# Kernel tuning notes

Measured on AMD Instinct MI355X. Metric: run time of the kernel, lower is better.

Reference implementation:

```python
import jax, jax.numpy as jnp
import numpy as np

EPS = 1e-6  # VNLeakyReLU eps
NORM_EPS = 1e-12  # F.normalize default eps
NEG_SLOPE = 0.2


def _normalize(v):
    # matches torch F.normalize(p=2, dim=-1): v / max(||v||, eps)
    n = jnp.linalg.norm(v, axis=-1, keepdims=True)
    return v / jnp.maximum(n, NORM_EPS)


def _bgs_extended(d6s):
    # d6s: [B,N,D,3,2] -> rotation matrices [B,N,D,3,3] (columns b1,b2,b3)
    b1 = _normalize(d6s[..., 0])
    a2 = d6s[..., 1]
    proj = jnp.sum(b1 * a2, axis=-1, keepdims=True) * b1
    b2 = _normalize(a2 - proj)
    b3 = jnp.cross(b1, b2)
    return jnp.stack([b1, b2, b3], axis=-1)


def setup_inputs() -> dict:
    key = jax.random.key(0)
    kX, kJ, kA, kB, kC, kW = jax.random.split(key, 6)
    B, N, Din, Dout = 8, 4096, 128, 256
    return {
        "X": jax.random.normal(kX, (B, N, Din, 3), dtype=jnp.float32),
        "J": jax.random.normal(kJ, (B, N, Din, 3, 2), dtype=jnp.float32),
        "Amat": jax.random.normal(kA, (Dout, Din), dtype=jnp.float32),
        "Bmat": jax.random.normal(kB, (Dout, Din), dtype=jnp.float32),
        "Cmat": jax.random.normal(kC, (Dout, Din), dtype=jnp.float32),
        "Wdir": jax.random.normal(kW, (Dout, Dout), dtype=jnp.float32),
        "device": 0,
    }


def reference(X, J, Amat, Bmat, Cmat, Wdir, device):
    # ---- Affine_Linear_Abla_wocomplex ----
    R = _bgs_extended(J)  # [B,N,D,3,3]
    # get_rtx(k, RT, X) = sum_j R[...,j,k] * X[...,j]; stacking k=0,1,2 gives:
    a_term = jnp.einsum('bndjk,bndj->bndk', R, X)  # [B,N,D,3]
    # Y = A@a + B@a + C@a == (A+B+C)@a  (einsum 'fe,bcei->bcfi')
    Y = jnp.einsum('fe,bnei->bnfi', Amat + Bmat + Cmat, a_term)  # [B,N,F,3]
    # ---- permute(0,2,3,1) -> [B, F, 3, N] ----
    x = jnp.transpose(Y, (0, 2, 3, 1))
    # ---- VNLeakyReLU ----
    d = jnp.einsum('oc,bcin->boin', Wdir, x)
    dot = jnp.sum(x * d, axis=2, keepdims=True)
    mask = (dot >= 0).astype(x.dtype)
    d_norm_sq = jnp.sum(d * d, axis=2, keepdims=True)
    x_out = NEG_SLOPE * x + (1 - NEG_SLOPE) * (
        mask * x + (1 - mask) * (x - dot / (d_norm_sq + EPS) * d)
    )
    return x_out  # [B, F, 3, N]
```

## Files before the change

kernel.cpp:

```cpp
#include <hip/hip_runtime.h>

#define TT 16
#define NBLK 2048
#define LDA 136

typedef short s16x8 __attribute__((ext_vector_type(8)));
typedef float f32x4 __attribute__((ext_vector_type(4)));

#define SCHED_FENCE() __builtin_amdgcn_sched_barrier(0)

__device__ __forceinline__ unsigned short f2bf(float f) {
  union { float f; unsigned u; } v; v.f = f;
  unsigned r = v.u + 0x7FFFu + ((v.u >> 16) & 1u);
  return (unsigned short)(r >> 16);
}
__device__ __forceinline__ float bf2f(unsigned short h) {
  union { unsigned u; float f; } v; v.u = ((unsigned)h) << 16;
  return v.f;
}
__device__ __forceinline__ void split2(float x, unsigned short& h, unsigned short& m) {
  h = f2bf(x);
  m = f2bf(x - bf2f(h));
}

__global__ __launch_bounds__(256) void prep1_kernel(
    const float* __restrict__ A, const float* __restrict__ Bm,
    const float* __restrict__ C,
    float* __restrict__ M3f,
    unsigned short* __restrict__ M3h, unsigned short* __restrict__ M3m) {
  int tid = blockIdx.x * 256 + threadIdx.x;
  float s = A[tid] + Bm[tid] + C[tid];
  M3f[tid] = s;
  unsigned short h, m;
  split2(s, h, m);
  M3h[tid] = h; M3m[tid] = m;
}

__global__ __launch_bounds__(256) void prep2_kernel(
    const float* __restrict__ W, const float* __restrict__ M3f,
    unsigned short* __restrict__ WMh, unsigned short* __restrict__ WMm) {
  __shared__ float wrow[256];
  __shared__ float part[128];
  const int o = blockIdx.x;
  const int t = threadIdx.x;
  const int e = t & 127;
  const int h = t >> 7;
  wrow[t] = W[o * 256 + t];
  __syncthreads();
  float dot = 0.f;
  const int c0 = h * 128;
  #pragma unroll 8
  for (int c = c0; c < c0 + 128; ++c) dot += wrow[c] * M3f[c * 128 + e];
  if (h) part[e] = dot;
  __syncthreads();
  if (!h) {
    float d = dot + part[e];
    unsigned short hh, mm;
    split2(d, hh, mm);
    WMh[o * 128 + e] = hh; WMm[o * 128 + e] = mm;
  }
}

#define B1LOADS(slot, ks) { \
  b1h[slot][0] = *(const s16x8*)(M3h + fB + (ks) * 32); \
  b1m[slot][0] = *(const s16x8*)(M3m + fB + (ks) * 32); \
  b1h[slot][1] = *(const s16x8*)(M3h + fB + 2048 + (ks) * 32); \
  b1m[slot][1] = *(const s16x8*)(M3m + fB + 2048 + (ks) * 32); }

#define WMLOADS(slot, ks) { \
  wmh[slot][0] = *(const s16x8*)(WMh + fB + (ks) * 32); \
  wmm[slot][0] = *(const s16x8*)(WMm + fB + (ks) * 32); \
  wmh[slot][1] = *(const s16x8*)(WMh + fB + 2048 + (ks) * 32); \
  wmm[slot][1] = *(const s16x8*)(WMm + fB + 2048 + (ks) * 32); }

#define GSTEPS(slot, ks) { \
  const int e0 = (ks) * 32 + quad * 8; \
  _Pragma("unroll") \
  for (int mt = 0; mt < 3; ++mt) { \
    s16x8 ah = *(const s16x8*)(aTh + (mt * 16 + nl) * LDA + e0); \
    s16x8 am = *(const s16x8*)(aTm + (mt * 16 + nl) * LDA + e0); \
    _Pragma("unroll") \
    for (int nt = 0; nt < 2; ++nt) { \
      f32x4 a1 = acc1[mt][nt]; \
      f32x4 a2 = acc2[mt][nt]; \
      a1 = __builtin_amdgcn_mfma_f32_16x16x32_bf16(ah, b1h[slot][nt], a1, 0, 0, 0); \
      a2 = __builtin_amdgcn_mfma_f32_16x16x32_bf16(ah, wmh[slot][nt], a2, 0, 0, 0); \
      a1 = __builtin_amdgcn_mfma_f32_16x16x32_bf16(ah, b1m[slot][nt], a1, 0, 0, 0); \
      a2 = __builtin_amdgcn_mfma_f32_16x16x32_bf16(ah, wmm[slot][nt], a2, 0, 0, 0); \
      a1 = __builtin_amdgcn_mfma_f32_16x16x32_bf16(am, b1h[slot][nt], a1, 0, 0, 0); \
      a2 = __builtin_amdgcn_mfma_f32_16x16x32_bf16(am, wmh[slot][nt], a2, 0, 0, 0); \
      acc1[mt][nt] = a1; acc2[mt][nt] = a2; \
    } \
  } }

__global__ __launch_bounds__(512, 3) void affine_vnrelu_mfma(
    const float* __restrict__ X, const float* __restrict__ J,
    const unsigned short* __restrict__ M3h, const unsigned short* __restrict__ M3m,
    const unsigned short* __restrict__ WMh, const unsigned short* __restrict__ WMm,
    float* __restrict__ out) {
  __shared__ unsigned short smem[2 * 48 * LDA];
  unsigned short* aTh = smem;
  unsigned short* aTm = smem + 48 * LDA;

  const int tid = threadIdx.x;
  const int lane = tid & 63;
  const int w = tid >> 6;
  const int quad = lane >> 4;
  const int nl = lane & 15;
  const long g0 = (long)blockIdx.x * TT;
  const int b = (int)(g0 >> 12);
  const int n0 = (int)(g0 & 4095);
  const int f0 = w * 32;
  const int fB = (f0 + nl) * 128 + quad * 8;
  const f32x4 zz = {0.f, 0.f, 0.f, 0.f};

  s16x8 b1h[2][2], b1m[2][2];
  s16x8 wmh[2][2], wmm[2][2];
  B1LOADS(0, 0); WMLOADS(0, 0);
  SCHED_FENCE();

  {
    int t = tid >> 5;
    int dch0 = (tid & 31) * 4;
    const float* Xp = X + ((g0 + t) * 128 + dch0) * 3;
    const float* Jp = J + ((g0 + t) * 128 + dch0) * 6;
    float xf[12], jf[24];
    #pragma unroll
    for (int q = 0; q < 3; ++q) *(float4*)(xf + 4 * q) = ((const float4*)Xp)[q];
    #pragma unroll
    for (int q = 0; q < 6; ++q) *(float4*)(jf + 4 * q) = ((const float4*)Jp)[q];

    unsigned short hs[3][4], ms[3][4];
    #pragma unroll
    for (int e = 0; e < 4; ++e) {
      float x0 = xf[3 * e], x1 = xf[3 * e + 1], x2 = xf[3 * e + 2];
      float j0 = jf[6 * e],     j1 = jf[6 * e + 1], j2 = jf[6 * e + 2];
      float j3 = jf[6 * e + 3], j4 = jf[6 * e + 4], j5 = jf[6 * e + 5];
      float c00 = j0, c01 = j2, c02 = j4;
      float a20 = j1, a21 = j3, a22 = j5;
      float nsq1 = c00 * c00 + c01 * c01 + c02 * c02;
      float inv1 = __builtin_amdgcn_rsqf(fmaxf(nsq1, 1e-24f));
      float b10 = c00 * inv1, b11 = c01 * inv1, b12 = c02 * inv1;
      float pr = b10 * a20 + b11 * a21 + b12 * a22;
      float u0 = a20 - pr * b10, u1 = a21 - pr * b11, u2 = a22 - pr * b12;
      float nsq2 = u0 * u0 + u1 * u1 + u2 * u2;
      float inv2 = __builtin_amdgcn_rsqf(fmaxf(nsq2, 1e-24f));
      float b20 = u0 * inv2, b21 = u1 * inv2, b22 = u2 * inv2;
      float b30 = b11 * b22 - b12 * b21;
      float b31 = b12 * b20 - b10 * b22;
      float b32 = b10 * b21 - b11 * b20;
      split2(b10 * x0 + b11 * x1 + b12 * x2, hs[0][e], ms[0][e]);
      split2(b20 * x0 + b21 * x1 + b22 * x2, hs[1][e], ms[1][e]);
      split2(b30 * x0 + b31 * x1 + b32 * x2, hs[2][e], ms[2][e]);
    }
    #pragma unroll
    for (int i = 0; i < 3; ++i) {
      short4 vh, vm;
      vh.x = hs[i][0]; vh.y = hs[i][1]; vh.z = hs[i][2]; vh.w = hs[i][3];
      vm.x = ms[i][0]; vm.y = ms[i][1]; vm.z = ms[i][2]; vm.w = ms[i][3];
      int ro = (i * 16 + t) * LDA + dch0;
      *(short4*)(aTh + ro) = vh;
      *(short4*)(aTm + ro) = vm;
    }
  }
  __syncthreads();

  f32x4 acc1[3][2], acc2[3][2];
  #pragma unroll
  for (int mt = 0; mt < 3; ++mt)
    #pragma unroll
    for (int nt = 0; nt < 2; ++nt) { acc1[mt][nt] = zz; acc2[mt][nt] = zz; }

  B1LOADS(1, 1); WMLOADS(1, 1);
  SCHED_FENCE();
  GSTEPS(0, 0);
  B1LOADS(0, 2); WMLOADS(0, 2);
  SCHED_FENCE();
  GSTEPS(1, 1);
  B1LOADS(1, 3); WMLOADS(1, 3);
  SCHED_FENCE();
  GSTEPS(0, 2);
  GSTEPS(1, 3);

  #pragma unroll
  for (int nt = 0; nt < 2; ++nt) {
    int f = f0 + nt * 16 + nl;
    float* ob = out + ((long)(b * 256 + f) * 3) * 4096 + n0 + quad * 4;
    float o[3][4];
    #pragma unroll
    for (int r = 0; r < 4; ++r) {
      float x0 = acc1[0][nt][r], x1 = acc1[1][nt][r], x2 = acc1[2][nt][r];
      float d0 = acc2[0][nt][r], d1 = acc2[1][nt][r], d2 = acc2[2][nt][r];
      float dot = x0 * d0 + x1 * d1 + x2 * d2;
      float dn = d0 * d0 + d1 * d1 + d2 * d2;
      float s = (dot < 0.0f) ? (0.8f * dot * __builtin_amdgcn_rcpf(dn + 1e-6f))
                             : 0.0f;
      o[0][r] = x0 - s * d0;
      o[1][r] = x1 - s * d1;
      o[2][r] = x2 - s * d2;
    }
    #pragma unroll
    for (int i = 0; i < 3; ++i)
      *(float4*)(ob + ((long)i * 4096)) = make_float4(o[i][0], o[i][1], o[i][2], o[i][3]);
  }
}

extern "C" void kernel_launch(void* const* d_in, const int* in_sizes, int n_in,
                              void* d_out, int out_size, void* d_ws, size_t ws_size,
                              hipStream_t stream) {
  const float* X = (const float*)d_in[0];
  const float* J = (const float*)d_in[1];
  const float* A = (const float*)d_in[2];
  const float* B = (const float*)d_in[3];
  const float* C = (const float*)d_in[4];
  const float* W = (const float*)d_in[5];
  unsigned short* M3h = (unsigned short*)d_ws;
  unsigned short* M3m = M3h + 128 * 256;
  unsigned short* WMh = M3m + 128 * 256;
  unsigned short* WMm = WMh + 128 * 256;
  float* M3f = (float*)(WMm + 128 * 256);
  float* out = (float*)d_out;

  prep1_kernel<<<128, 256, 0, stream>>>(A, B, C, M3f, M3h, M3m);
  prep2_kernel<<<256, 256, 0, stream>>>(W, M3f, WMh, WMm);
  affine_vnrelu_mfma<<<NBLK, 512, 0, stream>>>(
      X, J, M3h, M3m, WMh, WMm, out);
}
```

Before: 280.1 us.

## Make GEMM kernel persistent over 8 tiles with prefetched X/J loads

Each block now processes 8 consecutive 16-point tiles instead of one, with a grid of 256 blocks. The X and J loads for the next tile are issued before the current tile's MFMA work so their latency overlaps compute. Launch bounds drop to 2 blocks per SM to make room for the extra prefetch registers. The costs are fewer resident waves, extra barriers between tiles, and a grid of 256 blocks that may leave CUs idle on a 256-CU part at only 2 waves of work per block.

Result: no change. 278.5 us (-0.6%).

```diff
diff --git a/kernel.cpp b/kernel.cpp
--- a/kernel.cpp
+++ b/kernel.cpp
@@ -1,7 +1,8 @@
 #include <hip/hip_runtime.h>
 
 #define TT 16
-#define NBLK 2048
+#define NBLK 256
+#define NTILE 8
 #define LDA 136
 
 typedef short s16x8 __attribute__((ext_vector_type(8)));
@@ -93,7 +94,49 @@
     } \
   } }
 
-__global__ __launch_bounds__(512, 3) void affine_vnrelu_mfma(
+#define LOADXJ(g0t) { \
+  const float* Xp = X + (((g0t) + tA) * 128 + dch0) * 3; \
+  const float* Jp = J + (((g0t) + tA) * 128 + dch0) * 6; \
+  _Pragma("unroll") \
+  for (int q = 0; q < 3; ++q) *(float4*)(xf + 4 * q) = ((const float4*)Xp)[q]; \
+  _Pragma("unroll") \
+  for (int q = 0; q < 6; ++q) *(float4*)(jf + 4 * q) = ((const float4*)Jp)[q]; }
+
+#define GSPROC() { \
+  unsigned short hs[3][4], ms[3][4]; \
+  _Pragma("unroll") \
+  for (int e = 0; e < 4; ++e) { \
+    float x0 = xf[3 * e], x1 = xf[3 * e + 1], x2 = xf[3 * e + 2]; \
+    float j0 = jf[6 * e],     j1 = jf[6 * e + 1], j2 = jf[6 * e + 2]; \
+    float j3 = jf[6 * e + 3], j4 = jf[6 * e + 4], j5 = jf[6 * e + 5]; \
+    float c00 = j0, c01 = j2, c02 = j4; \
+    float a20 = j1, a21 = j3, a22 = j5; \
+    float nsq1 = c00 * c00 + c01 * c01 + c02 * c02; \
+    float inv1 = __builtin_amdgcn_rsqf(fmaxf(nsq1, 1e-24f)); \
+    float b10 = c00 * inv1, b11 = c01 * inv1, b12 = c02 * inv1; \
+    float pr = b10 * a20 + b11 * a21 + b12 * a22; \
+    float u0 = a20 - pr * b10, u1 = a21 - pr * b11, u2 = a22 - pr * b12; \
+    float nsq2 = u0 * u0 + u1 * u1 + u2 * u2; \
+    float inv2 = __builtin_amdgcn_rsqf(fmaxf(nsq2, 1e-24f)); \
+    float b20 = u0 * inv2, b21 = u1 * inv2, b22 = u2 * inv2; \
+    float b30 = b11 * b22 - b12 * b21; \
+    float b31 = b12 * b20 - b10 * b22; \
+    float b32 = b10 * b21 - b11 * b20; \
+    split2(b10 * x0 + b11 * x1 + b12 * x2, hs[0][e], ms[0][e]); \
+    split2(b20 * x0 + b21 * x1 + b22 * x2, hs[1][e], ms[1][e]); \
+    split2(b30 * x0 + b31 * x1 + b32 * x2, hs[2][e], ms[2][e]); \
+  } \
+  _Pragma("unroll") \
+  for (int i = 0; i < 3; ++i) { \
+    short4 vh, vm; \
+    vh.x = hs[i][0]; vh.y = hs[i][1]; vh.z = hs[i][2]; vh.w = hs[i][3]; \
+    vm.x = ms[i][0]; vm.y = ms[i][1]; vm.z = ms[i][2]; vm.w = ms[i][3]; \
+    int ro = (i * 16 + tA) * LDA + dch0; \
+    *(short4*)(aTh + ro) = vh; \
+    *(short4*)(aTm + ro) = vm; \
+  } }
+
+__global__ __launch_bounds__(512, 2) void affine_vnrelu_mfma(
     const float* __restrict__ X, const float* __restrict__ J,
     const unsigned short* __restrict__ M3h, const unsigned short* __restrict__ M3m,
     const unsigned short* __restrict__ WMh, const unsigned short* __restrict__ WMm,
@@ -107,101 +150,80 @@
   const int w = tid >> 6;
   const int quad = lane >> 4;
   const int nl = lane & 15;
-  const long g0 = (long)blockIdx.x * TT;
-  const int b = (int)(g0 >> 12);
-  const int n0 = (int)(g0 & 4095);
   const int f0 = w * 32;
   const int fB = (f0 + nl) * 128 + quad * 8;
+  const int tA = tid >> 5;
+  const int dch0 = (tid & 31) * 4;
   const f32x4 zz = {0.f, 0.f, 0.f, 0.f};
 
   s16x8 b1h[2][2], b1m[2][2];
   s16x8 wmh[2][2], wmm[2][2];
+  float xf[12], jf[24];
+
+  const long gbase = (long)blockIdx.x * NTILE * TT;
+
+  LOADXJ(gbase);
   B1LOADS(0, 0); WMLOADS(0, 0);
   SCHED_FENCE();
-
-  {
-    int t = tid >> 5;
-    int dch0 = (tid & 31) * 4;
-    const float* Xp = X + ((g0 + t) * 128 + dch0) * 3;
-    const float* Jp = J + ((g0 + t) * 128 + dch0) * 6;
-    float xf[12], jf[24];
+  GSPROC();
+  __syncthreads();
+
+  for (int it = 0; it < NTILE; ++it) {
+    const long g0c = gbase + (long)it * TT;
+
+    if (it + 1 < NTILE) { LOADXJ(g0c + TT); }
+    SCHED_FENCE();
+
+    f32x4 acc1[3][2], acc2[3][2];
     #pragma unroll
-    for (int q = 0; q < 3; ++q) *(float4*)(xf + 4 * q) = ((const float4*)Xp)[q];
-    #pragma unroll
-    for (int q = 0; q < 6; ++q) *(float4*)(jf + 4 * q) = ((const float4*)Jp)[q];
-
-    unsigned short hs[3][4], ms[3][4];
-    #pragma unroll
-    for (int e = 0; e < 4; ++e) {
-      float x0 = xf[3 * e], x1 = xf[3 * e + 1], x2 = xf[3 * e + 2];
-      float j0 = jf[6 * e],     j1 = jf[6 * e + 1], j2 = jf[6 * e + 2];
-      float j3 = jf[6 * e + 3], j4 = jf[6 * e + 4], j5 = jf[6 * e + 5];
-      float c00 = j0, c01 = j2, c02 = j4;
-      float a20 = j1, a21 = j3, a22 = j5;
-      float nsq1 = c00 * c00 + c01 * c01 + c02 * c02;
-      float inv1 = __builtin_amdgcn_rsqf(fmaxf(nsq1, 1e-24f));
-      float b10 = c00 * inv1, b11 = c01 * inv1, b12 = c02 * inv1;
-      float pr = b10 * a20 + b11 * a21 + b12 * a22;
-      float u0 = a20 - pr * b10, u1 = a21 - pr * b11, u2 = a22 - pr * b12;
-      float nsq2 = u0 * u0 + u1 * u1 + u2 * u2;
-      float inv2 = __builtin_amdgcn_rsqf(fmaxf(nsq2, 1e-24f));
-      float b20 = u0 * inv2, b21 = u1 * inv2, b22 = u2 * inv2;
-      float b30 = b11 * b22 - b12 * b21;
-      float b31 = b12 * b20 - b10 * b22;
-      float b32 = b10 * b21 - b11 * b20;
-      split2(b10 * x0 + b11 * x1 + b12 * x2, hs[0][e], ms[0][e]);
-      split2(b20 * x0 + b21 * x1 + b22 * x2, hs[1][e], ms[1][e]);
-      split2(b30 * x0 + b31 * x1 + b32 * x2, hs[2][e], ms[2][e]);
+    for (int mt = 0; mt < 3; ++mt)
+      #pragma unroll
+      for (int nt = 0; nt < 2; ++nt) { acc1[mt][nt] = zz; acc2[mt][nt] = zz; }
+
+    B1LOADS(1, 1); WMLOADS(1, 1);
+    SCHED_FENCE();
+    GSTEPS(0, 0);
+    B1LOADS(0, 2); WMLOADS(0, 2);
+    SCHED_FENCE();
+    GSTEPS(1, 1);
+    B1LOADS(1, 3); WMLOADS(1, 3);
+    SCHED_FENCE();
+    GSTEPS(0, 2);
+    GSTEPS(1, 3);
+
+    {
+      const int bb = (int)(g0c >> 12);
+      const int n0 = (int)(g0c & 4095);
+      #pragma unroll
+      for (int nt = 0; nt < 2; ++nt) {
+        int f = f0 + nt * 16 + nl;
+        float* ob = out + ((long)(bb * 256 + f) * 3) * 4096 + n0 + quad * 4;
+        float o[3][4];
+        #pragma unroll
+        for (int r = 0; r < 4; ++r) {
+          float x0 = acc1[0][nt][r], x1 = acc1[1][nt][r], x2 = acc1[2][nt][r];
+          float d0 = acc2[0][nt][r], d1 = acc2[1][nt][r], d2 = acc2[2][nt][r];
+          float dot = x0 * d0 + x1 * d1 + x2 * d2;
+          float dn = d0 * d0 + d1 * d1 + d2 * d2;
+          float s = (dot < 0.0f) ? (0.8f * dot * __builtin_amdgcn_rcpf(dn + 1e-6f))
+                                 : 0.0f;
+          o[0][r] = x0 - s * d0;
+          o[1][r] = x1 - s * d1;
+          o[2][r] = x2 - s * d2;
+        }
+        #pragma unroll
+        for (int i = 0; i < 3; ++i)
+          *(float4*)(ob + ((long)i * 4096)) = make_float4(o[i][0], o[i][1], o[i][2], o[i][3]);
+      }
     }
-    #pragma unroll
-    for (int i = 0; i < 3; ++i) {
-      short4 vh, vm;
-      vh.x = hs[i][0]; vh.y = hs[i][1]; vh.z = hs[i][2]; vh.w = hs[i][3];
-      vm.x = ms[i][0]; vm.y = ms[i][1]; vm.z = ms[i][2]; vm.w = ms[i][3];
-      int ro = (i * 16 + t) * LDA + dch0;
-      *(short4*)(aTh + ro) = vh;
-      *(short4*)(aTm + ro) = vm;
+
+    if (it + 1 < NTILE) {
+      __syncthreads();
+      B1LOADS(0, 0); WMLOADS(0, 0);
+      SCHED_FENCE();
+      GSPROC();
+      __syncthreads();
     }
-  }
-  __syncthreads();
-
-  f32x4 acc1[3][2], acc2[3][2];
-  #pragma unroll
-  for (int mt = 0; mt < 3; ++mt)
-    #pragma unroll
-    for (int nt = 0; nt < 2; ++nt) { acc1[mt][nt] = zz; acc2[mt][nt] = zz; }
-
-  B1LOADS(1, 1); WMLOADS(1, 1);
-  SCHED_FENCE();
-  GSTEPS(0, 0);
-  B1LOADS(0, 2); WMLOADS(0, 2);
-  SCHED_FENCE();
-  GSTEPS(1, 1);
-  B1LOADS(1, 3); WMLOADS(1, 3);
-  SCHED_FENCE();
-  GSTEPS(0, 2);
-  GSTEPS(1, 3);
-
-  #pragma unroll
-  for (int nt = 0; nt < 2; ++nt) {
-    int f = f0 + nt * 16 + nl;
-    float* ob = out + ((long)(b * 256 + f) * 3) * 4096 + n0 + quad * 4;
-    float o[3][4];
-    #pragma unroll
-    for (int r = 0; r < 4; ++r) {
-      float x0 = acc1[0][nt][r], x1 = acc1[1][nt][r], x2 = acc1[2][nt][r];
-      float d0 = acc2[0][nt][r], d1 = acc2[1][nt][r], d2 = acc2[2][nt][r];
-      float dot = x0 * d0 + x1 * d1 + x2 * d2;
-      float dn = d0 * d0 + d1 * d1 + d2 * d2;
-      float s = (dot < 0.0f) ? (0.8f * dot * __builtin_amdgcn_rcpf(dn + 1e-6f))
-                             : 0.0f;
-      o[0][r] = x0 - s * d0;
-      o[1][r] = x1 - s * d1;
-      o[2][r] = x2 - s * d2;
-    }
-    #pragma unroll
-    for (int i = 0; i < 3; ++i)
-      *(float4*)(ob + ((long)i * 4096)) = make_float4(o[i][0], o[i][1], o[i][2], o[i][3]);
   }
 }
 
```
